# Kernel optimization log

Measured on AMD Instinct MI355X. Metric: run time of the kernel, lower is better.

Reference implementation:

```python
import jax, jax.numpy as jnp
import numpy as np

D = 256      # d_model
SUB = 3      # number of adjacency subsets
GROUPS = 8
N, T, V = 32, 256, 19


def setup_inputs() -> dict:
    key = jax.random.key(0)
    ks = jax.random.split(key, 4)
    return {
        "x": jax.random.normal(ks[0], (N, T, V, D), jnp.float32),
        "para": jax.random.normal(ks[1], (3, GROUPS, V, V), jnp.float32),
        "linear_weight": jax.random.normal(ks[2], (D, D * SUB), jnp.float32) * 0.05,
        "linear_bias": jax.random.normal(ks[3], (1, D * SUB, 1, 1), jnp.float32) * 0.05,
        "bn_gamma": jnp.ones((D * SUB,), jnp.float32),
        "bn_beta": jnp.zeros((D * SUB,), jnp.float32),
        "bn1_gamma": jnp.ones((D,), jnp.float32),
        "bn1_beta": jnp.zeros((D,), jnp.float32),
    }


def _bn(x, gamma, beta, eps=1e-5):
    # BatchNorm2d (training mode): stats over (n, t, v) per channel
    m = jnp.mean(x, axis=(0, 2, 3), keepdims=True)
    v = jnp.var(x, axis=(0, 2, 3), keepdims=True)
    return (x - m) * jax.lax.rsqrt(v + eps) * gamma[None, :, None, None] + beta[None, :, None, None]


def reference(x, para, linear_weight, linear_bias, bn_gamma, bn_beta, bn1_gamma, bn1_beta):
    xc = jnp.transpose(x, (0, 3, 1, 2))                 # (n, c, t, v)
    # expand per-group adjacency to per-channel: (3, D, V, V)
    A = jnp.tile(para, (1, D // GROUPS, 1, 1))
    # L2 row-normalize along last dim (matches torch.norm(dim=-1))
    A = A / (jnp.linalg.norm(A, axis=-1, keepdims=True) + 1e-4)
    # channel mixing: (n, 3c, t, v)
    y = jnp.einsum('nctw,cd->ndtw', xc, linear_weight)
    y = _bn(y + linear_bias, bn_gamma, bn_beta)
    n, kc, t, v = y.shape
    y = y.reshape(n, SUB, kc // SUB, t, v)              # (n, k, c, t, v)
    # per-channel tiny 19x19 adjacency matmul
    y = jnp.einsum('nkctv,kcvw->nctw', y, A)            # (n, c, t, v)
    out = jax.nn.relu(_bn(y + xc, bn1_gamma, bn1_beta))
    return jnp.transpose(out, (0, 2, 3, 1))             # (n, t, v, c)
```

## Files before the change

### kernel.cpp

```cpp
#include <hip/hip_runtime.h>

typedef unsigned short u16;
typedef unsigned int u32;
typedef float f32x4 __attribute__((ext_vector_type(4)));
typedef __bf16 bf16x8 __attribute__((ext_vector_type(8)));

#define M_ALL 155648.0f
#define GP 168

__device__ __forceinline__ u16 f2bf(float f) {
  union { float f; u32 u; } x; x.f = f;
  u32 u = x.u;
  u += 0x7FFFu + ((u >> 16) & 1u);
  return (u16)(u >> 16);
}
__device__ __forceinline__ float bf2f(u16 h) {
  union { u32 u; float f; } x; x.u = ((u32)h) << 16;
  return x.f;
}
__device__ __forceinline__ f32x4 zero4() { f32x4 z = {0.f, 0.f, 0.f, 0.f}; return z; }

__device__ __forceinline__ int xs_idx(int m, int c) {
  return m * 256 + ((((c >> 3) ^ (m & 7)) << 3) | (c & 7));
}
__device__ __forceinline__ int y2_idx(int r, int kvp) {
  int sw = (r & 7) ^ ((r >> 3) & 7);
  return r * 64 + ((((kvp >> 3) ^ sw) << 3) | (kvp & 7));
}

__global__ void k_prep(const float* __restrict__ para, u16* __restrict__ wa2) {
  __shared__ float aL[3 * 8 * 19 * 19];
  int tid = threadIdx.x;
  if (tid < 456) {
    int k = tid / 152, rem = tid % 152, g = rem / 19, v = rem % 19;
    int base = ((k * 8 + g) * 19 + v) * 19;
    float ss = 0.f;
    #pragma unroll
    for (int w = 0; w < 19; ++w) { float a = para[base + w]; ss += a * a; }
    float inv = 1.f / (sqrtf(ss) + 1e-4f);
    #pragma unroll
    for (int w = 0; w < 19; ++w) aL[base + w] = para[base + w] * inv;
  }
  __syncthreads();
  for (int i = tid; i < 8 * 20 * 64; i += 512) {
    int g = i / 1280, rem = i % 1280, w = rem >> 6, kvp = rem & 63;
    u16 val = 0;
    if (w < 19 && kvp < 57) {
      int k = kvp / 19, v = kvp - 19 * k;
      val = f2bf(aL[((k * 8 + g) * 19 + v) * 19 + w]);
    }
    wa2[i] = val;
  }
}

__global__ void k_wt(const float* __restrict__ W, u16* __restrict__ wt) {
  int idx = blockIdx.x * 512 + threadIdx.x;
  int d = idx >> 8, c = idx & 255;
  wt[idx] = f2bf(W[c * 768 + d]);
}

__global__ __launch_bounds__(512, 2) void k_gram(const float* __restrict__ x,
                                                 float* __restrict__ G,
                                                 float* __restrict__ colsum) {
  __shared__ u16 xsT[256 * GP];
  __shared__ float scs[512];
  int tid = threadIdx.x, bid = blockIdx.x;
  int c = tid & 255, mh = tid >> 8;
  int lane = tid & 63, wave = tid >> 6;
  int cl = lane & 15, q = lane >> 4;

  if (tid < 256) {
    *reinterpret_cast<uint2*>(&xsT[tid * GP + 152]) = make_uint2(0u, 0u);
    *reinterpret_cast<uint2*>(&xsT[tid * GP + 156]) = make_uint2(0u, 0u);
  }

  float cs = 0.f;
  f32x4 acc[2][16];
  #pragma unroll
  for (int ri = 0; ri < 2; ++ri)
    #pragma unroll
    for (int j = 0; j < 16; ++j) acc[ri][j] = zero4();

  for (int ss = 0; ss < 4; ++ss) {
    int sl = bid * 4 + ss;
    const float* xb = x + (size_t)sl * 152 * 256;
    __syncthreads();
    #pragma unroll 1
    for (int it = 0; it < 19; ++it) {
      int m0 = it * 8 + mh * 4;
      float v0 = xb[(m0 + 0) * 256 + c];
      float v1 = xb[(m0 + 1) * 256 + c];
      float v2 = xb[(m0 + 2) * 256 + c];
      float v3 = xb[(m0 + 3) * 256 + c];
      cs += v0 + v1 + v2 + v3;
      uint2 p;
      p.x = (u32)f2bf(v0) | ((u32)f2bf(v1) << 16);
      p.y = (u32)f2bf(v2) | ((u32)f2bf(v3) << 16);
      *reinterpret_cast<uint2*>(&xsT[c * GP + m0]) = p;
    }
    __syncthreads();
    #pragma unroll
    for (int s = 0; s < 5; ++s) {
      int kof = s * 32 + q * 8;
      bf16x8 a0 = *reinterpret_cast<const bf16x8*>(&xsT[(wave * 16 + cl) * GP + kof]);
      bf16x8 a1 = *reinterpret_cast<const bf16x8*>(&xsT[((wave + 8) * 16 + cl) * GP + kof]);
      #pragma unroll
      for (int ct2 = 0; ct2 < 16; ++ct2) {
        bf16x8 b = *reinterpret_cast<const bf16x8*>(&xsT[(ct2 * 16 + cl) * GP + kof]);
        acc[0][ct2] = __builtin_amdgcn_mfma_f32_16x16x32_bf16(a0, b, acc[0][ct2], 0, 0, 0);
        acc[1][ct2] = __builtin_amdgcn_mfma_f32_16x16x32_bf16(a1, b, acc[1][ct2], 0, 0, 0);
      }
    }
  }
  #pragma unroll
  for (int ri = 0; ri < 2; ++ri) {
    int ct = wave + ri * 8;
    #pragma unroll
    for (int ct2 = 0; ct2 < 16; ++ct2) {
      if (ct2 >= ct) {
        #pragma unroll
        for (int r4 = 0; r4 < 4; ++r4)
          atomicAdd(&G[(ct * 16 + q * 4 + r4) * 256 + ct2 * 16 + cl], acc[ri][ct2][r4]);
      }
    }
  }
  scs[tid] = cs;
  __syncthreads();
  if (tid < 256) atomicAdd(&colsum[tid], scs[tid] + scs[tid + 256]);
}

__global__ void k_sym(float* __restrict__ G) {
  int i = blockIdx.x * 256 + threadIdx.x;
  int r = i >> 8, cN = i & 255;
  if (r > cN) G[i] = G[cN * 256 + r];
}

__global__ __launch_bounds__(256) void k_f1(const float* __restrict__ G,
                                            const float* __restrict__ colsum,
                                            const float* __restrict__ W,
                                            const float* __restrict__ gam,
                                            const float* __restrict__ bet,
                                            float* __restrict__ ST) {
  __shared__ float wd[256];
  __shared__ float red[16];
  int d = blockIdx.x, c = threadIdx.x;
  float wv = W[c * 768 + d];
  wd[c] = wv;
  __syncthreads();
  float dot = 0.f;
  const float* Gr = G + c * 256;
  #pragma unroll 4
  for (int j = 0; j < 256; ++j) dot += Gr[j] * wd[j];
  float part = wv * dot;
  float mpart = colsum[c] * wv;
  #pragma unroll
  for (int o = 32; o; o >>= 1) { part += __shfl_down(part, o); mpart += __shfl_down(mpart, o); }
  int lane = c & 63, w = c >> 6;
  if (lane == 0) { red[w] = part; red[8 + w] = mpart; }
  __syncthreads();
  if (c == 0) {
    float qv = red[0] + red[1] + red[2] + red[3];
    float ms = red[8] + red[9] + red[10] + red[11];
    float mean = ms / M_ALL;
    float var = qv / M_ALL - mean * mean;
    float S = gam[d] * rsqrtf(var + 1e-5f);
    ST[d] = S;
    ST[768 + d] = bet[d] - mean * S;
  }
}

__global__ __launch_bounds__(512, 2) void k_main(const float* __restrict__ x,
                                                 const u16* __restrict__ wt,
                                                 const u16* __restrict__ wa2,
                                                 const float* __restrict__ ST,
                                                 float* __restrict__ sumz,
                                                 float* __restrict__ out) {
  __shared__ u16 xs[152 * 256];
  __shared__ u16 y2[512 * 64];
  __shared__ float scrz[1024];
  int tid = threadIdx.x;
  int bid = blockIdx.x;
  const float* xbase = x + (size_t)bid * 152 * 256;
  size_t obase = (size_t)bid * 152 * 256;

  {
    int r = tid >> 6, c4 = (tid & 63) << 2;
    for (int it = 0; it < 19; ++it) {
      int m = it * 8 + r;
      float4 f = *reinterpret_cast<const float4*>(xbase + m * 256 + c4);
      uint2 p;
      p.x = (u32)f2bf(f.x) | ((u32)f2bf(f.y) << 16);
      p.y = (u32)f2bf(f.z) | ((u32)f2bf(f.w) << 16);
      *reinterpret_cast<uint2*>(&xs[xs_idx(m, c4)]) = p;
    }
  }

  int lane = tid & 63, wave = tid >> 6;
  int mhalf = wave & 1, nt3 = wave >> 1;
  int cl = lane & 15, q = lane >> 4;
  int g = wave;
  const bf16x8* wtv = reinterpret_cast<const bf16x8*>(wt);
  float* zbufF = reinterpret_cast<float*>(y2);

  bf16x8 bfr[2][2];
  #pragma unroll
  for (int ks = 0; ks < 2; ++ks)
    #pragma unroll
    for (int nt = 0; nt < 2; ++nt) {
      int w = nt * 16 + cl; int wc = (w < 20) ? w : 19;
      bfr[ks][nt] = *reinterpret_cast<const bf16x8*>(&wa2[(g * 20 + wc) * 64 + ks * 32 + q * 8]);
    }

  int arow[5], mlow[5];
  #pragma unroll
  for (int i = 0; i < 5; ++i) {
    int rr = mhalf * 80 + i * 16 + cl;
    if (rr > 151) rr = 151;
    arow[i] = rr * 256; mlow[i] = rr & 7;
  }
  __syncthreads();

  for (int nc = 0; nc < 4; ++nc) {
    f32x4 acc[5][3];
    #pragma unroll
    for (int i = 0; i < 5; ++i)
      #pragma unroll
      for (int jj = 0; jj < 3; ++jj) acc[i][jj] = zero4();
    for (int s = 0; s < 8; ++s) {
      int sq4 = s * 4 + q;
      bf16x8 b[3];
      #pragma unroll
      for (int jj = 0; jj < 3; ++jj) {
        int j = nt3 * 3 + jj;
        int d = (j >> 2) * 256 + nc * 64 + (j & 3) * 16 + cl;
        b[jj] = wtv[d * 32 + sq4];
      }
      #pragma unroll
      for (int i = 0; i < 5; ++i) {
        bf16x8 a = *reinterpret_cast<const bf16x8*>(&xs[arow[i] + ((sq4 ^ mlow[i]) << 3)]);
        #pragma unroll
        for (int jj = 0; jj < 3; ++jj)
          acc[i][jj] = __builtin_amdgcn_mfma_f32_16x16x32_bf16(a, b[jj], acc[i][jj], 0, 0, 0);
      }
    }
    __syncthreads();

    #pragma unroll
    for (int kk = 0; kk < 7; ++kk)
      y2[y2_idx(tid, 57 + kk)] = 0;

    #pragma unroll
    for (int jj = 0; jj < 3; ++jj) {
      int j = nt3 * 3 + jj;
      int ksub = j >> 2;
      int c_local = (j & 3) * 16 + cl;
      int d = ksub * 256 + nc * 64 + c_local;
      float Sc = ST[d], Tc = ST[768 + d];
      #pragma unroll
      for (int i = 0; i < 5; ++i) {
        int mb = mhalf * 80 + i * 16 + q * 4;
        #pragma unroll
        for (int r4 = 0; r4 < 4; ++r4) {
          int m = mb + r4;
          if (m < 152) {
            int t = (m * 27) >> 9;
            int v = m - t * 19;
            int kvp = ksub * 19 + v;
            int r = t * 64 + c_local;
            y2[y2_idx(r, kvp)] = f2bf(acc[i][jj][r4] * Sc + Tc);
          }
        }
      }
    }
    __syncthreads();

    f32x4 zacc[4][2];
    #pragma unroll
    for (int mt = 0; mt < 4; ++mt) { zacc[mt][0] = zero4(); zacc[mt][1] = zero4(); }
    #pragma unroll
    for (int ks = 0; ks < 2; ++ks) {
      #pragma unroll
      for (int mt = 0; mt < 4; ++mt) {
        int tc = mt * 16 + cl;
        int t = tc >> 3, c8 = tc & 7;
        int r = t * 64 + c8 * 8 + g;
        int ch = (ks * 4 + q) ^ g ^ c8;
        bf16x8 afr = *reinterpret_cast<const bf16x8*>(&y2[r * 64 + (ch << 3)]);
        #pragma unroll
        for (int nt = 0; nt < 2; ++nt)
          zacc[mt][nt] = __builtin_amdgcn_mfma_f32_16x16x32_bf16(afr, bfr[ks][nt], zacc[mt][nt], 0, 0, 0);
      }
    }
    __syncthreads();

    #pragma unroll
    for (int mt = 0; mt < 4; ++mt)
      #pragma unroll
      for (int nt = 0; nt < 2; ++nt) {
        int w = nt * 16 + cl;
        if (w < 19) {
          #pragma unroll
          for (int r4 = 0; r4 < 4; ++r4) {
            int mm = mt * 16 + q * 4 + r4;
            int t = mm >> 3, c8 = mm & 7;
            zbufF[(c8 * 8 + g) * 153 + t * 19 + w] = zacc[mt][nt][r4];
          }
        }
      }
    __syncthreads();

    float sz = 0.f, sq = 0.f;
    int cloc = tid & 63;
    int cglob = nc * 64 + cloc;
    #pragma unroll 1
    for (int rep = 0; rep < 19; ++rep) {
      int mp = rep * 8 + (tid >> 6);
      float z = zbufF[cloc * 153 + mp] + bf2f(xs[xs_idx(mp, cglob)]);
      out[obase + (size_t)mp * 256 + cglob] = z;
      sz += z; sq += z * z;
    }
    scrz[(tid >> 6) * 64 + cloc] = sz;
    scrz[512 + (tid >> 6) * 64 + cloc] = sq;
    __syncthreads();
    if (tid < 128) {
      int comp = tid >> 6, c = tid & 63;
      float v = 0.f;
      #pragma unroll
      for (int h = 0; h < 8; ++h) v += scrz[comp * 512 + h * 64 + c];
      atomicAdd(&sumz[comp * 256 + nc * 64 + c], v);
    }
  }
}

__global__ void k_f2(const float* __restrict__ statz, const float* __restrict__ gam,
                     const float* __restrict__ bet, float* __restrict__ S1T1) {
  int c = threadIdx.x;
  float inv = 1.f / M_ALL;
  float mz = statz[c] * inv;
  float qv = statz[256 + c] * inv;
  float var = qv - mz * mz;
  float Sc = gam[c] * rsqrtf(var + 1e-5f);
  S1T1[c] = Sc;
  S1T1[256 + c] = bet[c] - mz * Sc;
}

__global__ __launch_bounds__(256) void k_relu(float* __restrict__ out,
                                              const float* __restrict__ S1T1) {
  int tid = threadIdx.x;
  int lane = tid & 63;
  int wv = ((blockIdx.x << 8) + tid) >> 6;
  const float4* s14 = reinterpret_cast<const float4*>(S1T1);
  float4 sv = s14[lane], tv = s14[64 + lane];
  float4* o4 = reinterpret_cast<float4*>(out);
  #pragma unroll 1
  for (int r = 0; r < 19; ++r) {
    size_t i = ((size_t)r * 8192 + wv) * 64 + lane;
    float4 f = o4[i];
    f.x = fmaxf(f.x * sv.x + tv.x, 0.f);
    f.y = fmaxf(f.y * sv.y + tv.y, 0.f);
    f.z = fmaxf(f.z * sv.z + tv.z, 0.f);
    f.w = fmaxf(f.w * sv.w + tv.w, 0.f);
    o4[i] = f;
  }
}

extern "C" void kernel_launch(void* const* d_in, const int* in_sizes, int n_in,
                              void* d_out, int out_size, void* d_ws, size_t ws_size,
                              hipStream_t stream) {
  const float* x    = (const float*)d_in[0];
  const float* para = (const float*)d_in[1];
  const float* W    = (const float*)d_in[2];
  const float* bng  = (const float*)d_in[4];
  const float* bnb  = (const float*)d_in[5];
  const float* bn1g = (const float*)d_in[6];
  const float* bn1b = (const float*)d_in[7];
  float* out = (float*)d_out;

  char* ws = (char*)d_ws;
  u16* wt     = (u16*)ws;
  u16* wa2    = (u16*)(ws + 393216);
  float* G    = (float*)(ws + 413696);
  float* csum = (float*)(ws + 675840);
  float* sumz = (float*)(ws + 676864);
  float* ST   = (float*)(ws + 678912);
  float* S1T1 = (float*)(ws + 685056);

  hipMemsetAsync(ws + 413696, 0, 262144 + 1024 + 2048, stream);
  k_prep<<<dim3(1),    dim3(512), 0, stream>>>(para, wa2);
  k_wt  <<<dim3(384),  dim3(512), 0, stream>>>(W, wt);
  k_gram<<<dim3(256),  dim3(512), 0, stream>>>(x, G, csum);
  k_sym <<<dim3(256),  dim3(256), 0, stream>>>(G);
  k_f1  <<<dim3(768),  dim3(256), 0, stream>>>(G, csum, W, bng, bnb, ST);
  k_main<<<dim3(1024), dim3(512), 0, stream>>>(x, wt, wa2, ST, sumz, out);
  k_f2  <<<dim3(1),    dim3(256), 0, stream>>>(sumz, bn1g, bn1b, S1T1);
  k_relu<<<dim3(2048), dim3(256), 0, stream>>>(out, S1T1);
}
```

Before: 628.8 us.

## Halve k_main tile to 4 timesteps per block and widen k_gram loads

```diff
diff --git a/kernel.cpp b/kernel.cpp
--- a/kernel.cpp
+++ b/kernel.cpp
@@ -81,22 +81,26 @@
     #pragma unroll
     for (int j = 0; j < 16; ++j) acc[ri][j] = zero4();
 
+  int nit = mh ? 9 : 10;
+  int mbase = mh * 80;
+
   for (int ss = 0; ss < 4; ++ss) {
-    int sl = bid * 4 + ss;
-    const float* xb = x + (size_t)sl * 152 * 256;
-    __syncthreads();
-    #pragma unroll 1
-    for (int it = 0; it < 19; ++it) {
-      int m0 = it * 8 + mh * 4;
-      float v0 = xb[(m0 + 0) * 256 + c];
-      float v1 = xb[(m0 + 1) * 256 + c];
-      float v2 = xb[(m0 + 2) * 256 + c];
-      float v3 = xb[(m0 + 3) * 256 + c];
-      cs += v0 + v1 + v2 + v3;
-      uint2 p;
-      p.x = (u32)f2bf(v0) | ((u32)f2bf(v1) << 16);
-      p.y = (u32)f2bf(v2) | ((u32)f2bf(v3) << 16);
-      *reinterpret_cast<uint2*>(&xsT[c * GP + m0]) = p;
+    const float* xb = x + (size_t)(bid * 4 + ss) * 152 * 256;
+    __syncthreads();
+    #pragma unroll 2
+    for (int it = 0; it < nit; ++it) {
+      int m0 = mbase + it * 8;
+      float v[8];
+      #pragma unroll
+      for (int j = 0; j < 8; ++j) v[j] = xb[(m0 + j) * 256 + c];
+      #pragma unroll
+      for (int j = 0; j < 8; ++j) cs += v[j];
+      uint4 p;
+      p.x = (u32)f2bf(v[0]) | ((u32)f2bf(v[1]) << 16);
+      p.y = (u32)f2bf(v[2]) | ((u32)f2bf(v[3]) << 16);
+      p.z = (u32)f2bf(v[4]) | ((u32)f2bf(v[5]) << 16);
+      p.w = (u32)f2bf(v[6]) | ((u32)f2bf(v[7]) << 16);
+      *reinterpret_cast<uint4*>(&xsT[c * GP + m0]) = p;
     }
     __syncthreads();
     #pragma unroll
@@ -169,29 +173,32 @@
   }
 }
 
-__global__ __launch_bounds__(512, 2) void k_main(const float* __restrict__ x,
+__global__ __launch_bounds__(512, 4) void k_main(const float* __restrict__ x,
                                                  const u16* __restrict__ wt,
                                                  const u16* __restrict__ wa2,
                                                  const float* __restrict__ ST,
                                                  float* __restrict__ sumz,
                                                  float* __restrict__ out) {
-  __shared__ u16 xs[152 * 256];
-  __shared__ u16 y2[512 * 64];
+  __shared__ u16 xs[76 * 256];
+  __shared__ u16 y2[256 * 64];
   __shared__ float scrz[1024];
   int tid = threadIdx.x;
   int bid = blockIdx.x;
-  const float* xbase = x + (size_t)bid * 152 * 256;
-  size_t obase = (size_t)bid * 152 * 256;
+  const float* xbase = x + (size_t)bid * 76 * 256;
+  size_t obase = (size_t)bid * 76 * 256;
 
   {
     int r = tid >> 6, c4 = (tid & 63) << 2;
-    for (int it = 0; it < 19; ++it) {
+    #pragma unroll
+    for (int it = 0; it < 10; ++it) {
       int m = it * 8 + r;
-      float4 f = *reinterpret_cast<const float4*>(xbase + m * 256 + c4);
-      uint2 p;
-      p.x = (u32)f2bf(f.x) | ((u32)f2bf(f.y) << 16);
-      p.y = (u32)f2bf(f.z) | ((u32)f2bf(f.w) << 16);
-      *reinterpret_cast<uint2*>(&xs[xs_idx(m, c4)]) = p;
+      if (m < 76) {
+        float4 f = *reinterpret_cast<const float4*>(xbase + m * 256 + c4);
+        uint2 p;
+        p.x = (u32)f2bf(f.x) | ((u32)f2bf(f.y) << 16);
+        p.y = (u32)f2bf(f.z) | ((u32)f2bf(f.w) << 16);
+        *reinterpret_cast<uint2*>(&xs[xs_idx(m, c4)]) = p;
+      }
     }
   }
 
@@ -211,19 +218,20 @@
       bfr[ks][nt] = *reinterpret_cast<const bf16x8*>(&wa2[(g * 20 + wc) * 64 + ks * 32 + q * 8]);
     }
 
-  int arow[5], mlow[5];
+  int imax = mhalf ? 2 : 3;
+  int arow[3], mlow[3];
   #pragma unroll
-  for (int i = 0; i < 5; ++i) {
-    int rr = mhalf * 80 + i * 16 + cl;
-    if (rr > 151) rr = 151;
+  for (int i = 0; i < 3; ++i) {
+    int rr = mhalf * 48 + i * 16 + cl;
+    if (rr > 75) rr = 75;
     arow[i] = rr * 256; mlow[i] = rr & 7;
   }
   __syncthreads();
 
   for (int nc = 0; nc < 4; ++nc) {
-    f32x4 acc[5][3];
-    #pragma unroll
-    for (int i = 0; i < 5; ++i)
+    f32x4 acc[3][3];
+    #pragma unroll
+    for (int i = 0; i < 3; ++i)
       #pragma unroll
       for (int jj = 0; jj < 3; ++jj) acc[i][jj] = zero4();
     for (int s = 0; s < 8; ++s) {
@@ -235,8 +243,7 @@
         int d = (j >> 2) * 256 + nc * 64 + (j & 3) * 16 + cl;
         b[jj] = wtv[d * 32 + sq4];
       }
-      #pragma unroll
-      for (int i = 0; i < 5; ++i) {
+      for (int i = 0; i < imax; ++i) {
         bf16x8 a = *reinterpret_cast<const bf16x8*>(&xs[arow[i] + ((sq4 ^ mlow[i]) << 3)]);
         #pragma unroll
         for (int jj = 0; jj < 3; ++jj)
@@ -245,9 +252,11 @@
     }
     __syncthreads();
 
-    #pragma unroll
-    for (int kk = 0; kk < 7; ++kk)
-      y2[y2_idx(tid, 57 + kk)] = 0;
+    if (tid < 256) {
+      #pragma unroll
+      for (int kk = 0; kk < 7; ++kk)
+        y2[y2_idx(tid, 57 + kk)] = 0;
+    }
 
     #pragma unroll
     for (int jj = 0; jj < 3; ++jj) {
@@ -256,13 +265,12 @@
       int c_local = (j & 3) * 16 + cl;
       int d = ksub * 256 + nc * 64 + c_local;
       float Sc = ST[d], Tc = ST[768 + d];
-      #pragma unroll
-      for (int i = 0; i < 5; ++i) {
-        int mb = mhalf * 80 + i * 16 + q * 4;
+      for (int i = 0; i < imax; ++i) {
+        int mb = mhalf * 48 + i * 16 + q * 4;
         #pragma unroll
         for (int r4 = 0; r4 < 4; ++r4) {
           int m = mb + r4;
-          if (m < 152) {
+          if (m < 76) {
             int t = (m * 27) >> 9;
             int v = m - t * 19;
             int kvp = ksub * 19 + v;
@@ -274,13 +282,13 @@
     }
     __syncthreads();
 
-    f32x4 zacc[4][2];
-    #pragma unroll
-    for (int mt = 0; mt < 4; ++mt) { zacc[mt][0] = zero4(); zacc[mt][1] = zero4(); }
+    f32x4 zacc[2][2];
+    #pragma unroll
+    for (int mt = 0; mt < 2; ++mt) { zacc[mt][0] = zero4(); zacc[mt][1] = zero4(); }
     #pragma unroll
     for (int ks = 0; ks < 2; ++ks) {
       #pragma unroll
-      for (int mt = 0; mt < 4; ++mt) {
+      for (int mt = 0; mt < 2; ++mt) {
         int tc = mt * 16 + cl;
         int t = tc >> 3, c8 = tc & 7;
         int r = t * 64 + c8 * 8 + g;
@@ -294,7 +302,7 @@
     __syncthreads();
 
     #pragma unroll
-    for (int mt = 0; mt < 4; ++mt)
+    for (int mt = 0; mt < 2; ++mt)
       #pragma unroll
       for (int nt = 0; nt < 2; ++nt) {
         int w = nt * 16 + cl;
@@ -303,7 +311,7 @@
           for (int r4 = 0; r4 < 4; ++r4) {
             int mm = mt * 16 + q * 4 + r4;
             int t = mm >> 3, c8 = mm & 7;
-            zbufF[(c8 * 8 + g) * 153 + t * 19 + w] = zacc[mt][nt][r4];
+            zbufF[(c8 * 8 + g) * 77 + t * 19 + w] = zacc[mt][nt][r4];
           }
         }
       }
@@ -313,11 +321,13 @@
     int cloc = tid & 63;
     int cglob = nc * 64 + cloc;
     #pragma unroll 1
-    for (int rep = 0; rep < 19; ++rep) {
+    for (int rep = 0; rep < 10; ++rep) {
       int mp = rep * 8 + (tid >> 6);
-      float z = zbufF[cloc * 153 + mp] + bf2f(xs[xs_idx(mp, cglob)]);
-      out[obase + (size_t)mp * 256 + cglob] = z;
-      sz += z; sq += z * z;
+      if (mp < 76) {
+        float z = zbufF[cloc * 77 + mp] + bf2f(xs[xs_idx(mp, cglob)]);
+        out[obase + (size_t)mp * 256 + cglob] = z;
+        sz += z; sq += z * z;
+      }
     }
     scrz[(tid >> 6) * 64 + cloc] = sz;
     scrz[512 + (tid >> 6) * 64 + cloc] = sq;
@@ -391,7 +401,7 @@
   k_gram<<<dim3(256),  dim3(512), 0, stream>>>(x, G, csum);
   k_sym <<<dim3(256),  dim3(256), 0, stream>>>(G);
   k_f1  <<<dim3(768),  dim3(256), 0, stream>>>(G, csum, W, bng, bnb, ST);
-  k_main<<<dim3(1024), dim3(512), 0, stream>>>(x, wt, wa2, ST, sumz, out);
+  k_main<<<dim3(2048), dim3(512), 0, stream>>>(x, wt, wa2, ST, sumz, out);
   k_f2  <<<dim3(1),    dim3(256), 0, stream>>>(sumz, bn1g, bn1b, S1T1);
   k_relu<<<dim3(2048), dim3(256), 0, stream>>>(out, S1T1);
 }
```

After: 1.707 ms. 2.72x slower.
